# Kernel tuning notes

Hardware: AMD Instinct MI355X
Metric: run time of the kernel (lower is better)

Reference implementation:

```python
import jax, jax.numpy as jnp
import numpy as np

COMMITMENT_COST = 0.25
NUM_CODES = 1024   # module's embedding_dim arg (K)
CODE_DIM = 512     # module's num_embeddings arg (D)


def setup_inputs() -> dict:
    key = jax.random.key(0)
    k1, k2 = jax.random.split(key)
    latents = jax.random.normal(k1, (64, 512, 512), dtype=jnp.float32)
    # torch init: uniform_(-1/K, 1/K)
    codebook = jax.random.uniform(
        k2, (NUM_CODES, CODE_DIM), dtype=jnp.float32,
        minval=-1.0 / NUM_CODES, maxval=1.0 / NUM_CODES)
    return {"continous_latents": latents, "codebook": codebook}


def reference(continous_latents, codebook):
    latents_shape = continous_latents.shape
    flat = continous_latents.reshape(-1, codebook.shape[1])        # [N, D]
    # squared Euclidean distances (argmin-equivalent to torch.cdist)
    d2 = (jnp.sum(flat * flat, axis=1, keepdims=True)
          - 2.0 * flat @ codebook.T
          + jnp.sum(codebook * codebook, axis=1))                  # [N, K]
    enc_idx = jnp.argmin(d2, axis=1)                               # [N]
    quantized = codebook[enc_idx].reshape(latents_shape)           # gather == one-hot matmul
    commitment_loss = jnp.mean(
        (jax.lax.stop_gradient(quantized) - continous_latents) ** 2)
    embedding_loss = jnp.mean(
        (quantized - jax.lax.stop_gradient(continous_latents)) ** 2)
    vq_loss = embedding_loss + COMMITMENT_COST * commitment_loss
    # straight-through estimator
    quantized_st = continous_latents + jax.lax.stop_gradient(
        quantized - continous_latents)
    return (quantized_st, vq_loss)
```

## Files before the change

kernel.cpp:

```cpp
#include <hip/hip_runtime.h>
#include <cfloat>

#define LAT_ROWS 32768
#define DIM 512
#define KCODES 1024

constexpr int BM = 64;
constexpr int BN = 256;
constexpr int BK = 64;
constexpr int NT = 512;
constexpr int NCT = KCODES / BN;
constexpr int NDK = DIM / BK;
constexpr int TT = NCT * NDK;
constexpr int CUNITS = BN * BK / 8;

constexpr size_t WS_LSUM = 0;
constexpr size_t WS_NORM = 512;
constexpr size_t WS_CBF8 = 4608;
constexpr size_t WS_XF8  = 4608 + 524288;
constexpr size_t WS_NEEDED = WS_XF8 + (size_t)LAT_ROWS * DIM;

typedef float f32x4 __attribute__((ext_vector_type(4)));
typedef short bf16x8 __attribute__((ext_vector_type(8)));
typedef unsigned short u16;
typedef u16 u16x8 __attribute__((ext_vector_type(8)));

__device__ __forceinline__ u16 f2bf(float f) {
  unsigned u = __float_as_uint(f);
  u += 0x7FFF + ((u >> 16) & 1);
  return (u16)(u >> 16);
}

__device__ __forceinline__ int2 pk8_fp8(const float4 a, const float4 c) {
  int lo = __builtin_amdgcn_cvt_pk_fp8_f32(a.x, a.y, 0, false);
  lo = __builtin_amdgcn_cvt_pk_fp8_f32(a.z, a.w, lo, true);
  int hi = __builtin_amdgcn_cvt_pk_fp8_f32(c.x, c.y, 0, false);
  hi = __builtin_amdgcn_cvt_pk_fp8_f32(c.z, c.w, hi, true);
  int2 v; v.x = lo; v.y = hi;
  return v;
}

#define GLOAD_LDS(g, l)                                     \
  __builtin_amdgcn_global_load_lds(                         \
      (const __attribute__((address_space(1))) void*)(g),   \
      (__attribute__((address_space(3))) void*)(l), 16, 0, 0)

__global__ void __launch_bounds__(NT)
vq_prep(const float* __restrict__ X, const float* __restrict__ CB,
        long* __restrict__ Xf8, long* __restrict__ CBf8,
        float* __restrict__ norms, double* __restrict__ lsum) {
  __shared__ float sp[8];
  const int bb = blockIdx.x;
  const int tid = threadIdx.x;
  if (bb < 4096) {
    const int id = bb * NT + tid;
    const int l15 = id & 15;
    const int l4 = (id >> 4) & 3;
    const int ks = (id >> 6) & 1;
    const int nf = (id >> 7) & 1;
    const int wn = (id >> 8) & 1;
    const int dk = (id >> 9) & 7;
    const int b = id >> 12;
    const int r = b * 64 + wn * 32 + nf * 16 + l15;
    const int d0 = dk * 64 + ks * 32 + l4 * 8;
    const float* src = X + (size_t)r * DIM + d0;
    const float4 a = *(const float4*)src;
    const float4 c = *(const float4*)(src + 4);
    float s = a.x * a.x + a.y * a.y + a.z * a.z + a.w * a.w +
              c.x * c.x + c.y * c.y + c.z * c.z + c.w * c.w;
    *(int2*)(Xf8 + id) = pk8_fp8(a, c);
#pragma unroll
    for (int m = 1; m < 64; m <<= 1) s += __shfl_xor(s, m, 64);
    const int lane = tid & 63, w = tid >> 6;
    if (lane == 0) sp[w] = s;
    __syncthreads();
    if (tid == 0) {
      double t = 0.0;
      for (int i = 0; i < 8; ++i) t += (double)sp[i];
      atomicAdd(&lsum[bb & 63], t);
    }
  } else if (bb < 4224) {
    const int id = (bb - 4096) * NT + tid;
    const int ct = id >> 14;
    const int dk = (id >> 11) & 7;
    const int u = id & 2047;
    const int r = u >> 3, qp = u & 7, q = qp ^ (r & 7);
    const float* src = CB + ((size_t)ct * BN + r) * DIM + dk * BK + q * 8;
    const float4 a = *(const float4*)src;
    const float4 c = *(const float4*)(src + 4);
    *(int2*)(CBf8 + id) = pk8_fp8(a, c);
  } else {
    const int gw = (bb - 4224) * 8 + (tid >> 6);
    const int l = tid & 63;
    const float4 a = *(const float4*)&CB[(size_t)gw * DIM + l * 8];
    const float4 b = *(const float4*)&CB[(size_t)gw * DIM + l * 8 + 4];
    float s = a.x * a.x + a.y * a.y + a.z * a.z + a.w * a.w +
              b.x * b.x + b.y * b.y + b.z * b.z + b.w * b.w;
#pragma unroll
    for (int m = 1; m < 64; m <<= 1) s += __shfl_xor(s, m, 64);
    if (l == 0) norms[gw] = s;
  }
}

__global__ void __launch_bounds__(NT, 4)
vq_main9(const long* __restrict__ Xf8, const long* __restrict__ CBf8,
         const float* __restrict__ CB, const float* __restrict__ norms,
         float* __restrict__ outq, double* __restrict__ lsum) {
  __shared__ long Cs[2][CUNITS];
  __shared__ float snorm[KCODES];
  __shared__ float redm[BM][4];
  __shared__ int redi[BM][4];
  __shared__ int idxs[BM];
  __shared__ float wpart[8];

  const int tid = threadIdx.x;
  const int lane = tid & 63;
  const int l15 = lane & 15;
  const int l4 = lane >> 4;
  const int wid = tid >> 6;
  const int wm = wid & 3;
  const int wn = wid >> 2;
  const int b = blockIdx.x;
  const int row0 = b * BM;

  for (int i = tid; i < KCODES; i += NT) snorm[i] = norms[i];

  const long* xw = Xf8 + (size_t)b * 4096 + wn * 256 + lane;

  auto stage = [&](int bf, int t) {
    const int ct = t >> 3, dk = t & 7;
    const char* cp = (const char*)(CBf8 + (size_t)(ct * NDK + dk) * CUNITS);
    char* dst = (char*)&Cs[bf][0];
#pragma unroll
    for (int k = 0; k < 2; ++k) {
      const int o = (tid + k * NT) * 16;
      GLOAD_LDS(cp + o, dst + o);
    }
  };

  f32x4 acc[4][2];
  float rmin[2]; int ridx[2];
#pragma unroll
  for (int i = 0; i < 2; ++i) { rmin[i] = FLT_MAX; ridx[i] = 0; }

  stage(0, 0);
  __syncthreads();

  for (int t = 0; t < TT; ++t) {
    const int dk = t & 7;
    const int cur = t & 1;
    long bfr[2][2];
    const long* xp = xw + dk * 512;
#pragma unroll
    for (int ks = 0; ks < 2; ++ks)
#pragma unroll
      for (int nf = 0; nf < 2; ++nf)
        bfr[ks][nf] = xp[nf * 128 + ks * 64];
    if (t + 1 < TT) stage(cur ^ 1, t + 1);

    if (dk == 0) {
      const f32x4 z = {0.f, 0.f, 0.f, 0.f};
#pragma unroll
      for (int mf = 0; mf < 4; ++mf)
#pragma unroll
        for (int nf = 0; nf < 2; ++nf) acc[mf][nf] = z;
    }
#pragma unroll
    for (int ks = 0; ks < 2; ++ks) {
      long af[4];
#pragma unroll
      for (int mf = 0; mf < 4; ++mf) {
        const int r = wm * 64 + mf * 16 + l15;
        const int ph = (ks * 4 + l4) ^ (r & 7);
        af[mf] = Cs[cur][r * 8 + ph];
      }
      __builtin_amdgcn_s_setprio(1);
#pragma unroll
      for (int mf = 0; mf < 4; ++mf)
#pragma unroll
        for (int nf = 0; nf < 2; ++nf)
          acc[mf][nf] = __builtin_amdgcn_mfma_f32_16x16x32_fp8_fp8(
              af[mf], bfr[ks][nf], acc[mf][nf], 0, 0, 0);
      __builtin_amdgcn_s_setprio(0);
    }
    if (dk == NDK - 1) {
      const int ct = t >> 3;
#pragma unroll
      for (int mf = 0; mf < 4; ++mf) {
#pragma unroll
        for (int r = 0; r < 4; ++r) {
          const int code = ct * BN + wm * 64 + mf * 16 + l4 * 4 + r;
          const float cn = snorm[code];
#pragma unroll
          for (int nf = 0; nf < 2; ++nf) {
            const float s = fmaf(-2.f, acc[mf][nf][r], cn);
            if (s < rmin[nf]) { rmin[nf] = s; ridx[nf] = code; }
          }
        }
      }
    }
    __syncthreads();
  }

#pragma unroll
  for (int m = 16; m <= 32; m <<= 1) {
#pragma unroll
    for (int nf = 0; nf < 2; ++nf) {
      const float om = __shfl_xor(rmin[nf], m, 64);
      const int oi = __shfl_xor(ridx[nf], m, 64);
      if (om < rmin[nf] || (om == rmin[nf] && oi < ridx[nf])) {
        rmin[nf] = om; ridx[nf] = oi;
      }
    }
  }
  if (l4 == 0) {
#pragma unroll
    for (int nf = 0; nf < 2; ++nf) {
      const int row = wn * 32 + nf * 16 + l15;
      redm[row][wm] = rmin[nf];
      redi[row][wm] = ridx[nf];
    }
  }
  __syncthreads();

  float tot = 0.f;
  if (tid < BM) {
    float bm = redm[tid][0]; int bi = redi[tid][0];
#pragma unroll
    for (int c = 1; c < 4; ++c) {
      const float m_ = redm[tid][c]; const int i_ = redi[tid][c];
      if (m_ < bm || (m_ == bm && i_ < bi)) { bm = m_; bi = i_; }
    }
    idxs[tid] = bi;
    tot = bm;
  }
#pragma unroll
  for (int m = 1; m < 64; m <<= 1) tot += __shfl_xor(tot, m, 64);
  if (lane == 0) wpart[wid] = tot;
  __syncthreads();
  if (tid == 0) {
    double s = 0.0;
    for (int i = 0; i < 8; ++i) s += (double)wpart[i];
    atomicAdd(&lsum[blockIdx.x & 63], s);
  }

  for (int g = tid; g < BM * (DIM / 4); g += NT) {
    const int row = g >> 7;
    const int d4 = (g & 127) * 4;
    const int idx = idxs[row];
    *(float4*)&outq[(size_t)(row0 + row) * DIM + d4] =
        *(const float4*)&CB[(size_t)idx * DIM + d4];
  }
}

constexpr int FBM = 128, FBN = 256, FBK = 64, FNT = 512, FNDK = 8, FTT = 32;

__global__ void __launch_bounds__(FNT, 2)
vq_main_fb(const float* __restrict__ X, const float* __restrict__ CB,
           const float* __restrict__ norms, float* __restrict__ outq,
           double* __restrict__ lsum) {
  __shared__ u16 Xs[2][FBM * FBK];
  __shared__ u16 Cs[2][FBN * FBK];
  __shared__ float snorm[KCODES];
  __shared__ float redm[FBM][4];
  __shared__ int redi[FBM][4];
  __shared__ int idxs[FBM];
  __shared__ float wpart[8];

  const int tid = threadIdx.x;
  const int lane = tid & 63;
  const int l15 = lane & 15;
  const int l4 = lane >> 4;
  const int wid = tid >> 6;
  const int wm = wid & 3;
  const int wn = wid >> 2;
  const int row0 = blockIdx.x * FBM;

  for (int i = tid; i < KCODES; i += FNT) snorm[i] = norms[i];

  int xlds[2]; const float* xbase[2];
#pragma unroll
  for (int k = 0; k < 2; ++k) {
    const int u = tid + k * FNT;
    const int r = u >> 3, q = u & 7, ph = q ^ (r & 7);
    xlds[k] = r * FBK + ph * 8;
    xbase[k] = X + (size_t)(row0 + r) * DIM + q * 8;
  }
  int clds[4]; const float* cbase[4];
#pragma unroll
  for (int k = 0; k < 4; ++k) {
    const int u = tid + k * FNT;
    const int r = u >> 3, q = u & 7, ph = q ^ (r & 7);
    clds[k] = r * FBK + ph * 8;
    cbase[k] = CB + (size_t)r * DIM + q * 8;
  }

  f32x4 acc[4][4];
  float rmin[4]; int ridx[4];
#pragma unroll
  for (int i = 0; i < 4; ++i) { rmin[i] = FLT_MAX; ridx[i] = 0; }
  float sq = 0.f;

  float4 lx[2][2], lc[4][2];
  auto load_tile = [&](int tn) {
    const int ct = tn >> 3, dk = tn & 7;
    const int xo = dk * FBK;
    const size_t co = (size_t)ct * FBN * DIM + dk * FBK;
#pragma unroll
    for (int k = 0; k < 2; ++k) {
      lx[k][0] = *(const float4*)(xbase[k] + xo);
      lx[k][1] = *(const float4*)(xbase[k] + xo + 4);
    }
#pragma unroll
    for (int k = 0; k < 4; ++k) {
      lc[k][0] = *(const float4*)(cbase[k] + co);
      lc[k][1] = *(const float4*)(cbase[k] + co + 4);
    }
  };
  auto write_tile = [&](int bb, bool acc_sq) {
#pragma unroll
    for (int k = 0; k < 2; ++k) {
      u16x8 v;
      const float* f = (const float*)&lx[k][0];
#pragma unroll
      for (int j = 0; j < 8; ++j) {
        const float x = f[j];
        if (acc_sq) sq = fmaf(x, x, sq);
        v[j] = f2bf(x);
      }
      *(u16x8*)&Xs[bb][xlds[k]] = v;
    }
#pragma unroll
    for (int k = 0; k < 4; ++k) {
      u16x8 v;
      const float* f = (const float*)&lc[k][0];
#pragma unroll
      for (int j = 0; j < 8; ++j) v[j] = f2bf(f[j]);
      *(u16x8*)&Cs[bb][clds[k]] = v;
    }
  };

  load_tile(0);
  write_tile(0, true);
  __syncthreads();

  int cur = 0;
  for (int t = 0; t < FTT; ++t) {
    const int dk = t & 7;
    const bool pre = (t + 1 < FTT);
    if (pre) load_tile(t + 1);
    if (dk == 0) {
      const f32x4 z = {0.f, 0.f, 0.f, 0.f};
#pragma unroll
      for (int mf = 0; mf < 4; ++mf)
#pragma unroll
        for (int nf = 0; nf < 4; ++nf) acc[mf][nf] = z;
    }
    const u16* xb = Xs[cur];
    const u16* cb = Cs[cur];
#pragma unroll
    for (int ks = 0; ks < 2; ++ks) {
      bf16x8 af[4], bfr[4];
#pragma unroll
      for (int mf = 0; mf < 4; ++mf) {
        const int r = wm * 64 + mf * 16 + l15;
        const int ph = (ks * 4 + l4) ^ (r & 7);
        af[mf] = *(const bf16x8*)&cb[r * FBK + ph * 8];
      }
#pragma unroll
      for (int nf = 0; nf < 4; ++nf) {
        const int r = wn * 64 + nf * 16 + l15;
        const int ph = (ks * 4 + l4) ^ (r & 7);
        bfr[nf] = *(const bf16x8*)&xb[r * FBK + ph * 8];
      }
#pragma unroll
      for (int mf = 0; mf < 4; ++mf)
#pragma unroll
        for (int nf = 0; nf < 4; ++nf)
          acc[mf][nf] = __builtin_amdgcn_mfma_f32_16x16x32_bf16(
              af[mf], bfr[nf], acc[mf][nf], 0, 0, 0);
    }
    if (dk == FNDK - 1) {
      const int ct = t >> 3;
#pragma unroll
      for (int mf = 0; mf < 4; ++mf) {
#pragma unroll
        for (int r = 0; r < 4; ++r) {
          const int code = ct * FBN + wm * 64 + mf * 16 + l4 * 4 + r;
          const float cn = snorm[code];
#pragma unroll
          for (int nf = 0; nf < 4; ++nf) {
            const float s = fmaf(-2.f, acc[mf][nf][r], cn);
            if (s < rmin[nf]) { rmin[nf] = s; ridx[nf] = code; }
          }
        }
      }
    }
    if (pre) write_tile(cur ^ 1, (t + 1) < FNDK);
    __syncthreads();
    cur ^= 1;
  }

#pragma unroll
  for (int m = 16; m <= 32; m <<= 1) {
#pragma unroll
    for (int nf = 0; nf < 4; ++nf) {
      const float om = __shfl_xor(rmin[nf], m, 64);
      const int oi = __shfl_xor(ridx[nf], m, 64);
      if (om < rmin[nf] || (om == rmin[nf] && oi < ridx[nf])) {
        rmin[nf] = om; ridx[nf] = oi;
      }
    }
  }
  if (l4 == 0) {
#pragma unroll
    for (int nf = 0; nf < 4; ++nf) {
      const int row = wn * 64 + nf * 16 + l15;
      redm[row][wm] = rmin[nf];
      redi[row][wm] = ridx[nf];
    }
  }
  __syncthreads();

  float tot = sq;
  if (tid < FBM) {
    float bm = redm[tid][0]; int bi = redi[tid][0];
#pragma unroll
    for (int c = 1; c < 4; ++c) {
      const float m_ = redm[tid][c]; const int i_ = redi[tid][c];
      if (m_ < bm || (m_ == bm && i_ < bi)) { bm = m_; bi = i_; }
    }
    idxs[tid] = bi;
    tot += bm;
  }
#pragma unroll
  for (int m = 1; m < 64; m <<= 1) tot += __shfl_xor(tot, m, 64);
  if (lane == 0) wpart[wid] = tot;
  __syncthreads();
  if (tid == 0) {
    double s = 0.0;
    for (int i = 0; i < 8; ++i) s += (double)wpart[i];
    atomicAdd(&lsum[blockIdx.x & 63], s);
  }

  for (int g = tid; g < FBM * (DIM / 4); g += FNT) {
    const int row = g >> 7;
    const int d4 = (g & 127) * 4;
    const int idx = idxs[row];
    *(float4*)&outq[(size_t)(row0 + row) * DIM + d4] =
        *(const float4*)&CB[(size_t)idx * DIM + d4];
  }
}

__global__ void vq_norms_kernel(const float* __restrict__ cb,
                                float* __restrict__ norms) {
  const int gw = (int)((blockIdx.x * blockDim.x + threadIdx.x) >> 6);
  const int l = threadIdx.x & 63;
  const float4 a = *(const float4*)&cb[(size_t)gw * DIM + l * 8];
  const float4 b = *(const float4*)&cb[(size_t)gw * DIM + l * 8 + 4];
  float s = a.x * a.x + a.y * a.y + a.z * a.z + a.w * a.w +
            b.x * b.x + b.y * b.y + b.z * b.z + b.w * b.w;
#pragma unroll
  for (int m = 1; m < 64; m <<= 1) s += __shfl_xor(s, m, 64);
  if (l == 0) norms[gw] = s;
}

__global__ void vq_finalize_kernel(const double* __restrict__ lsum,
                                   float* __restrict__ out) {
  double t = 0.0;
  for (int i = 0; i < 64; ++i) t += lsum[i];
  out[0] = (float)(1.25 * t / (double)((size_t)LAT_ROWS * DIM));
}

extern "C" void kernel_launch(void* const* d_in, const int* in_sizes, int n_in,
                              void* d_out, int out_size, void* d_ws, size_t ws_size,
                              hipStream_t stream) {
  const float* X = (const float*)d_in[0];
  const float* CB = (const float*)d_in[1];
  float* out = (float*)d_out;
  double* lsum = (double*)((char*)d_ws + WS_LSUM);
  float* norms = (float*)((char*)d_ws + WS_NORM);

  hipMemsetAsync(d_ws, 0, 512, stream);
  if (ws_size >= WS_NEEDED) {
    long* CBf8 = (long*)((char*)d_ws + WS_CBF8);
    long* Xf8 = (long*)((char*)d_ws + WS_XF8);
    vq_prep<<<4352, NT, 0, stream>>>(X, CB, Xf8, CBf8, norms, lsum);
    vq_main9<<<LAT_ROWS / BM, NT, 0, stream>>>(Xf8, CBf8, CB, norms, out, lsum);
  } else {
    vq_norms_kernel<<<KCODES / 4, 256, 0, stream>>>(CB, norms);
    vq_main_fb<<<LAT_ROWS / FBM, FNT, 0, stream>>>(X, CB, norms, out, lsum);
  }
  vq_finalize_kernel<<<1, 1, 0, stream>>>(lsum, out + (size_t)LAT_ROWS * DIM);
}
```

Baseline: 69.01 us.

## Double K-step per barrier in main loop and coalesce fp8 prep via LDS

The main kernel now stages two 64-wide K slices of the fp8 codebook per pipeline phase, which halves the number of barriers and stage calls while doubling LDS usage for the codebook buffer. The LDS swizzle changes from an XOR on the row to a rotation keyed on the lane's row index, and the codebook prep writes its layout to match. The latent prep kernel now has each block convert a whole 64-row tile with coalesced reads, permutes it through padded shared memory, and writes the fragment layout out contiguously, which cuts the block count from 4096 to 512. The larger LDS footprint could reduce occupancy.

```diff
diff --git a/kernel.cpp b/kernel.cpp
--- a/kernel.cpp
+++ b/kernel.cpp
@@ -11,7 +11,7 @@
 constexpr int NT = 512;
 constexpr int NCT = KCODES / BN;
 constexpr int NDK = DIM / BK;
-constexpr int TT = NCT * NDK;
+constexpr int NPH = 16;
 constexpr int CUNITS = BN * BK / 8;
 
 constexpr size_t WS_LSUM = 0;
@@ -49,26 +49,35 @@
 vq_prep(const float* __restrict__ X, const float* __restrict__ CB,
         long* __restrict__ Xf8, long* __restrict__ CBf8,
         float* __restrict__ norms, double* __restrict__ lsum) {
-  __shared__ float sp[8];
   const int bb = blockIdx.x;
   const int tid = threadIdx.x;
-  if (bb < 4096) {
-    const int id = bb * NT + tid;
-    const int l15 = id & 15;
-    const int l4 = (id >> 4) & 3;
-    const int ks = (id >> 6) & 1;
-    const int nf = (id >> 7) & 1;
-    const int wn = (id >> 8) & 1;
-    const int dk = (id >> 9) & 7;
-    const int b = id >> 12;
-    const int r = b * 64 + wn * 32 + nf * 16 + l15;
-    const int d0 = dk * 64 + ks * 32 + l4 * 8;
-    const float* src = X + (size_t)r * DIM + d0;
-    const float4 a = *(const float4*)src;
-    const float4 c = *(const float4*)(src + 4);
-    float s = a.x * a.x + a.y * a.y + a.z * a.z + a.w * a.w +
-              c.x * c.x + c.y * c.y + c.z * c.z + c.w * c.w;
-    *(int2*)(Xf8 + id) = pk8_fp8(a, c);
+  if (bb < 512) {
+    __shared__ long xl[4096 + 256];
+    __shared__ float sp[8];
+    float s = 0.f;
+#pragma unroll
+    for (int c = 0; c < 8; ++c) {
+      const int j = c * NT + tid;
+      const int r = j >> 6;
+      const int d0 = (j & 63) * 8;
+      const float* src = X + ((size_t)bb * BM + r) * DIM + d0;
+      const float4 a = *(const float4*)src;
+      const float4 cc = *(const float4*)(src + 4);
+      s += a.x * a.x + a.y * a.y + a.z * a.z + a.w * a.w +
+           cc.x * cc.x + cc.y * cc.y + cc.z * cc.z + cc.w * cc.w;
+      const int dk = d0 >> 6, ks = (d0 >> 5) & 1, l4 = (d0 >> 3) & 3;
+      const int wn = (r >> 5) & 1, nf = (r >> 4) & 1, l15 = r & 15;
+      const int unit = dk * 512 + wn * 256 + nf * 128 + ks * 64 + l4 * 16 + l15;
+      const int2 v = pk8_fp8(a, cc);
+      *(int2*)&xl[unit + (unit >> 4)] = v;
+    }
+    __syncthreads();
+    long* dst = Xf8 + (size_t)bb * 4096;
+#pragma unroll
+    for (int k = 0; k < 8; ++k) {
+      const int u = k * NT + tid;
+      dst[u] = xl[u + (u >> 4)];
+    }
 #pragma unroll
     for (int m = 1; m < 64; m <<= 1) s += __shfl_xor(s, m, 64);
     const int lane = tid & 63, w = tid >> 6;
@@ -79,18 +88,19 @@
       for (int i = 0; i < 8; ++i) t += (double)sp[i];
       atomicAdd(&lsum[bb & 63], t);
     }
-  } else if (bb < 4224) {
-    const int id = (bb - 4096) * NT + tid;
+  } else if (bb < 640) {
+    const int id = (bb - 512) * NT + tid;
     const int ct = id >> 14;
     const int dk = (id >> 11) & 7;
     const int u = id & 2047;
-    const int r = u >> 3, qp = u & 7, q = qp ^ (r & 7);
+    const int r = u >> 3, qp = u & 7;
+    const int q = (qp + 8 - ((r >> 1) & 7)) & 7;
     const float* src = CB + ((size_t)ct * BN + r) * DIM + dk * BK + q * 8;
     const float4 a = *(const float4*)src;
     const float4 c = *(const float4*)(src + 4);
     *(int2*)(CBf8 + id) = pk8_fp8(a, c);
   } else {
-    const int gw = (bb - 4224) * 8 + (tid >> 6);
+    const int gw = (bb - 640) * 8 + (tid >> 6);
     const int l = tid & 63;
     const float4 a = *(const float4*)&CB[(size_t)gw * DIM + l * 8];
     const float4 b = *(const float4*)&CB[(size_t)gw * DIM + l * 8 + 4];
@@ -103,10 +113,10 @@
 }
 
 __global__ void __launch_bounds__(NT, 4)
-vq_main9(const long* __restrict__ Xf8, const long* __restrict__ CBf8,
-         const float* __restrict__ CB, const float* __restrict__ norms,
-         float* __restrict__ outq, double* __restrict__ lsum) {
-  __shared__ long Cs[2][CUNITS];
+vq_main10(const long* __restrict__ Xf8, const long* __restrict__ CBf8,
+          const float* __restrict__ CB, const float* __restrict__ norms,
+          float* __restrict__ outq, double* __restrict__ lsum) {
+  __shared__ long Cs[2][2 * CUNITS];
   __shared__ float snorm[KCODES];
   __shared__ float redm[BM][4];
   __shared__ int redi[BM][4];
@@ -127,12 +137,12 @@
 
   const long* xw = Xf8 + (size_t)b * 4096 + wn * 256 + lane;
 
-  auto stage = [&](int bf, int t) {
-    const int ct = t >> 3, dk = t & 7;
-    const char* cp = (const char*)(CBf8 + (size_t)(ct * NDK + dk) * CUNITS);
+  auto stage = [&](int bf, int tt) {
+    const int ct = tt >> 2, pr = tt & 3;
+    const char* cp = (const char*)(CBf8 + (size_t)(ct * NDK + pr * 2) * CUNITS);
     char* dst = (char*)&Cs[bf][0];
 #pragma unroll
-    for (int k = 0; k < 2; ++k) {
+    for (int k = 0; k < 4; ++k) {
       const int o = (tid + k * NT) * 16;
       GLOAD_LDS(cp + o, dst + o);
     }
@@ -146,19 +156,22 @@
   stage(0, 0);
   __syncthreads();
 
-  for (int t = 0; t < TT; ++t) {
-    const int dk = t & 7;
-    const int cur = t & 1;
-    long bfr[2][2];
-    const long* xp = xw + dk * 512;
-#pragma unroll
-    for (int ks = 0; ks < 2; ++ks)
-#pragma unroll
-      for (int nf = 0; nf < 2; ++nf)
-        bfr[ks][nf] = xp[nf * 128 + ks * 64];
-    if (t + 1 < TT) stage(cur ^ 1, t + 1);
-
-    if (dk == 0) {
+  for (int tt = 0; tt < NPH; ++tt) {
+    const int pr = tt & 3;
+    const int cur = tt & 1;
+    long bfr[2][2][2];
+#pragma unroll
+    for (int dkp = 0; dkp < 2; ++dkp) {
+      const long* xp = xw + (pr * 2 + dkp) * 512;
+#pragma unroll
+      for (int ks = 0; ks < 2; ++ks)
+#pragma unroll
+        for (int nf = 0; nf < 2; ++nf)
+          bfr[dkp][ks][nf] = xp[nf * 128 + ks * 64];
+    }
+    if (tt + 1 < NPH) stage(cur ^ 1, tt + 1);
+
+    if (pr == 0) {
       const f32x4 z = {0.f, 0.f, 0.f, 0.f};
 #pragma unroll
       for (int mf = 0; mf < 4; ++mf)
@@ -166,25 +179,28 @@
         for (int nf = 0; nf < 2; ++nf) acc[mf][nf] = z;
     }
 #pragma unroll
-    for (int ks = 0; ks < 2; ++ks) {
-      long af[4];
-#pragma unroll
-      for (int mf = 0; mf < 4; ++mf) {
-        const int r = wm * 64 + mf * 16 + l15;
-        const int ph = (ks * 4 + l4) ^ (r & 7);
-        af[mf] = Cs[cur][r * 8 + ph];
-      }
-      __builtin_amdgcn_s_setprio(1);
-#pragma unroll
-      for (int mf = 0; mf < 4; ++mf)
-#pragma unroll
-        for (int nf = 0; nf < 2; ++nf)
-          acc[mf][nf] = __builtin_amdgcn_mfma_f32_16x16x32_fp8_fp8(
-              af[mf], bfr[ks][nf], acc[mf][nf], 0, 0, 0);
-      __builtin_amdgcn_s_setprio(0);
-    }
-    if (dk == NDK - 1) {
-      const int ct = t >> 3;
+    for (int dkp = 0; dkp < 2; ++dkp) {
+#pragma unroll
+      for (int ks = 0; ks < 2; ++ks) {
+        long af[4];
+#pragma unroll
+        for (int mf = 0; mf < 4; ++mf) {
+          const int r = wm * 64 + mf * 16 + l15;
+          const int ph = ((ks * 4 + l4) + (l15 >> 1)) & 7;
+          af[mf] = Cs[cur][dkp * CUNITS + r * 8 + ph];
+        }
+        __builtin_amdgcn_s_setprio(1);
+#pragma unroll
+        for (int mf = 0; mf < 4; ++mf)
+#pragma unroll
+          for (int nf = 0; nf < 2; ++nf)
+            acc[mf][nf] = __builtin_amdgcn_mfma_f32_16x16x32_fp8_fp8(
+                af[mf], bfr[dkp][ks][nf], acc[mf][nf], 0, 0, 0);
+        __builtin_amdgcn_s_setprio(0);
+      }
+    }
+    if (pr == 3) {
+      const int ct = tt >> 2;
 #pragma unroll
       for (int mf = 0; mf < 4; ++mf) {
 #pragma unroll
@@ -485,8 +501,8 @@
   if (ws_size >= WS_NEEDED) {
     long* CBf8 = (long*)((char*)d_ws + WS_CBF8);
     long* Xf8 = (long*)((char*)d_ws + WS_XF8);
-    vq_prep<<<4352, NT, 0, stream>>>(X, CB, Xf8, CBf8, norms, lsum);
-    vq_main9<<<LAT_ROWS / BM, NT, 0, stream>>>(Xf8, CBf8, CB, norms, out, lsum);
+    vq_prep<<<768, NT, 0, stream>>>(X, CB, Xf8, CBf8, norms, lsum);
+    vq_main10<<<LAT_ROWS / BM, NT, 0, stream>>>(Xf8, CBf8, CB, norms, out, lsum);
   } else {
     vq_norms_kernel<<<KCODES / 4, 256, 0, stream>>>(CB, norms);
     vq_main_fb<<<LAT_ROWS / FBM, FNT, 0, stream>>>(X, CB, norms, out, lsum);
```

After: 65.15 us. 5.6% less time.

## Fuse latent FP8 conversion into main kernel, stream codebook from global

Applied to the files above, without the earlier changes.

Drops the separate pass that converted all latents to FP8 in workspace. The main kernel now reads its 64-row fp32 tile of X directly, converts it to FP8 in a swizzled LDS layout, and accumulates the latent squared norm on the fly. Codebook fragments, pre-packed in MFMA register order, are loaded straight from global memory (L2-resident) instead of double-buffered through LDS, which removes the per-step barriers. This saves the 64 MB intermediate write and read, at the cost of exposing global-load latency inside the MFMA loop.

```diff
diff --git a/kernel.cpp b/kernel.cpp
--- a/kernel.cpp
+++ b/kernel.cpp
@@ -7,18 +7,14 @@
 
 constexpr int BM = 64;
 constexpr int BN = 256;
-constexpr int BK = 64;
 constexpr int NT = 512;
-constexpr int NCT = KCODES / BN;
-constexpr int NDK = DIM / BK;
-constexpr int TT = NCT * NDK;
-constexpr int CUNITS = BN * BK / 8;
+constexpr int NCT = 4;
+constexpr int NDK = 8;
 
 constexpr size_t WS_LSUM = 0;
 constexpr size_t WS_NORM = 512;
 constexpr size_t WS_CBF8 = 4608;
-constexpr size_t WS_XF8  = 4608 + 524288;
-constexpr size_t WS_NEEDED = WS_XF8 + (size_t)LAT_ROWS * DIM;
+constexpr size_t WS_NEEDED = WS_CBF8 + 65536 * 8;
 
 typedef float f32x4 __attribute__((ext_vector_type(4)));
 typedef short bf16x8 __attribute__((ext_vector_type(8)));
@@ -31,66 +27,39 @@
   return (u16)(u >> 16);
 }
 
-__device__ __forceinline__ int2 pk8_fp8(const float4 a, const float4 c) {
+__device__ __forceinline__ long pk8_fp8l(const float4 a, const float4 c) {
   int lo = __builtin_amdgcn_cvt_pk_fp8_f32(a.x, a.y, 0, false);
   lo = __builtin_amdgcn_cvt_pk_fp8_f32(a.z, a.w, lo, true);
   int hi = __builtin_amdgcn_cvt_pk_fp8_f32(c.x, c.y, 0, false);
   hi = __builtin_amdgcn_cvt_pk_fp8_f32(c.z, c.w, hi, true);
-  int2 v; v.x = lo; v.y = hi;
-  return v;
-}
-
-#define GLOAD_LDS(g, l)                                     \
-  __builtin_amdgcn_global_load_lds(                         \
-      (const __attribute__((address_space(1))) void*)(g),   \
-      (__attribute__((address_space(3))) void*)(l), 16, 0, 0)
+  return ((long)(unsigned)hi << 32) | (unsigned)lo;
+}
+
+__device__ __forceinline__ int xswz(int u) {
+  const int add = ((u >> 2) & 12) + ((u >> 5) & 2) + ((u >> 9) & 1);
+  return (u & ~15) | ((u + add) & 15);
+}
 
 __global__ void __launch_bounds__(NT)
-vq_prep(const float* __restrict__ X, const float* __restrict__ CB,
-        long* __restrict__ Xf8, long* __restrict__ CBf8,
-        float* __restrict__ norms, double* __restrict__ lsum) {
-  __shared__ float sp[8];
+vq_prep11(const float* __restrict__ CB, long* __restrict__ CBf8,
+          float* __restrict__ norms) {
   const int bb = blockIdx.x;
   const int tid = threadIdx.x;
-  if (bb < 4096) {
+  if (bb < 128) {
     const int id = bb * NT + tid;
-    const int l15 = id & 15;
-    const int l4 = (id >> 4) & 3;
-    const int ks = (id >> 6) & 1;
-    const int nf = (id >> 7) & 1;
-    const int wn = (id >> 8) & 1;
-    const int dk = (id >> 9) & 7;
-    const int b = id >> 12;
-    const int r = b * 64 + wn * 32 + nf * 16 + l15;
-    const int d0 = dk * 64 + ks * 32 + l4 * 8;
-    const float* src = X + (size_t)r * DIM + d0;
+    const int t = id >> 11;
+    const int r = id & 2047;
+    const int wm = r >> 9, mf = (r >> 7) & 3, ks = (r >> 6) & 1,
+              l4 = (r >> 4) & 3, l15 = id & 15;
+    const int ct = t >> 3, dk = t & 7;
+    const int code = ct * BN + wm * 64 + mf * 16 + l15;
+    const int d0 = dk * 64 + (ks * 4 + l4) * 8;
+    const float* src = CB + (size_t)code * DIM + d0;
     const float4 a = *(const float4*)src;
     const float4 c = *(const float4*)(src + 4);
-    float s = a.x * a.x + a.y * a.y + a.z * a.z + a.w * a.w +
-              c.x * c.x + c.y * c.y + c.z * c.z + c.w * c.w;
-    *(int2*)(Xf8 + id) = pk8_fp8(a, c);
-#pragma unroll
-    for (int m = 1; m < 64; m <<= 1) s += __shfl_xor(s, m, 64);
-    const int lane = tid & 63, w = tid >> 6;
-    if (lane == 0) sp[w] = s;
-    __syncthreads();
-    if (tid == 0) {
-      double t = 0.0;
-      for (int i = 0; i < 8; ++i) t += (double)sp[i];
-      atomicAdd(&lsum[bb & 63], t);
-    }
-  } else if (bb < 4224) {
-    const int id = (bb - 4096) * NT + tid;
-    const int ct = id >> 14;
-    const int dk = (id >> 11) & 7;
-    const int u = id & 2047;
-    const int r = u >> 3, qp = u & 7, q = qp ^ (r & 7);
-    const float* src = CB + ((size_t)ct * BN + r) * DIM + dk * BK + q * 8;
-    const float4 a = *(const float4*)src;
-    const float4 c = *(const float4*)(src + 4);
-    *(int2*)(CBf8 + id) = pk8_fp8(a, c);
+    CBf8[id] = pk8_fp8l(a, c);
   } else {
-    const int gw = (bb - 4224) * 8 + (tid >> 6);
+    const int gw = (bb - 128) * 8 + (tid >> 6);
     const int l = tid & 63;
     const float4 a = *(const float4*)&CB[(size_t)gw * DIM + l * 8];
     const float4 b = *(const float4*)&CB[(size_t)gw * DIM + l * 8 + 4];
@@ -103,10 +72,10 @@
 }
 
 __global__ void __launch_bounds__(NT, 4)
-vq_main9(const long* __restrict__ Xf8, const long* __restrict__ CBf8,
-         const float* __restrict__ CB, const float* __restrict__ norms,
-         float* __restrict__ outq, double* __restrict__ lsum) {
-  __shared__ long Cs[2][CUNITS];
+vq_main11(const float* __restrict__ X, const long* __restrict__ CBf8,
+          const float* __restrict__ CB, const float* __restrict__ norms,
+          float* __restrict__ outq, double* __restrict__ lsum) {
+  __shared__ long Xs[4096];
   __shared__ float snorm[KCODES];
   __shared__ float redm[BM][4];
   __shared__ int redi[BM][4];
@@ -125,40 +94,29 @@
 
   for (int i = tid; i < KCODES; i += NT) snorm[i] = norms[i];
 
-  const long* xw = Xf8 + (size_t)b * 4096 + wn * 256 + lane;
-
-  auto stage = [&](int bf, int t) {
-    const int ct = t >> 3, dk = t & 7;
-    const char* cp = (const char*)(CBf8 + (size_t)(ct * NDK + dk) * CUNITS);
-    char* dst = (char*)&Cs[bf][0];
-#pragma unroll
-    for (int k = 0; k < 2; ++k) {
-      const int o = (tid + k * NT) * 16;
-      GLOAD_LDS(cp + o, dst + o);
-    }
-  };
+  float sq = 0.f;
+#pragma unroll
+  for (int c = 0; c < 8; ++c) {
+    const int rl = c * 8 + wid;
+    const float* src = X + (size_t)(row0 + rl) * DIM + lane * 8;
+    const float4 a = *(const float4*)src;
+    const float4 d = *(const float4*)(src + 4);
+    sq += a.x * a.x + a.y * a.y + a.z * a.z + a.w * a.w +
+          d.x * d.x + d.y * d.y + d.z * d.z + d.w * d.w;
+    const int q = lane;
+    const int u = (q >> 3) * 512 + (rl >> 5) * 256 + ((rl >> 4) & 1) * 128 +
+                  ((q >> 2) & 1) * 64 + (q & 3) * 16 + (rl & 15);
+    Xs[xswz(u)] = pk8_fp8l(a, d);
+  }
+  __syncthreads();
 
   f32x4 acc[4][2];
   float rmin[2]; int ridx[2];
 #pragma unroll
   for (int i = 0; i < 2; ++i) { rmin[i] = FLT_MAX; ridx[i] = 0; }
 
-  stage(0, 0);
-  __syncthreads();
-
-  for (int t = 0; t < TT; ++t) {
-    const int dk = t & 7;
-    const int cur = t & 1;
-    long bfr[2][2];
-    const long* xp = xw + dk * 512;
-#pragma unroll
-    for (int ks = 0; ks < 2; ++ks)
-#pragma unroll
-      for (int nf = 0; nf < 2; ++nf)
-        bfr[ks][nf] = xp[nf * 128 + ks * 64];
-    if (t + 1 < TT) stage(cur ^ 1, t + 1);
-
-    if (dk == 0) {
+  for (int ct = 0; ct < NCT; ++ct) {
+    {
       const f32x4 z = {0.f, 0.f, 0.f, 0.f};
 #pragma unroll
       for (int mf = 0; mf < 4; ++mf)
@@ -166,40 +124,46 @@
         for (int nf = 0; nf < 2; ++nf) acc[mf][nf] = z;
     }
 #pragma unroll
-    for (int ks = 0; ks < 2; ++ks) {
-      long af[4];
-#pragma unroll
-      for (int mf = 0; mf < 4; ++mf) {
-        const int r = wm * 64 + mf * 16 + l15;
-        const int ph = (ks * 4 + l4) ^ (r & 7);
-        af[mf] = Cs[cur][r * 8 + ph];
-      }
+    for (int dk = 0; dk < NDK; ++dk) {
+      const long* cbt = CBf8 + ((ct * 8 + dk) * 2048 + wm * 512) + lane;
+      long af[2][4];
+#pragma unroll
+      for (int ks = 0; ks < 2; ++ks)
+#pragma unroll
+        for (int mf = 0; mf < 4; ++mf)
+          af[ks][mf] = cbt[mf * 128 + ks * 64];
+      long bfr[2][2];
+#pragma unroll
+      for (int ks = 0; ks < 2; ++ks)
+#pragma unroll
+        for (int nf = 0; nf < 2; ++nf) {
+          const int u = dk * 512 + wn * 256 + nf * 128 + ks * 64 + l4 * 16 + l15;
+          bfr[ks][nf] = Xs[xswz(u)];
+        }
       __builtin_amdgcn_s_setprio(1);
 #pragma unroll
-      for (int mf = 0; mf < 4; ++mf)
-#pragma unroll
-        for (int nf = 0; nf < 2; ++nf)
-          acc[mf][nf] = __builtin_amdgcn_mfma_f32_16x16x32_fp8_fp8(
-              af[mf], bfr[ks][nf], acc[mf][nf], 0, 0, 0);
+      for (int ks = 0; ks < 2; ++ks)
+#pragma unroll
+        for (int mf = 0; mf < 4; ++mf)
+#pragma unroll
+          for (int nf = 0; nf < 2; ++nf)
+            acc[mf][nf] = __builtin_amdgcn_mfma_f32_16x16x32_fp8_fp8(
+                af[ks][mf], bfr[ks][nf], acc[mf][nf], 0, 0, 0);
       __builtin_amdgcn_s_setprio(0);
     }
-    if (dk == NDK - 1) {
-      const int ct = t >> 3;
-#pragma unroll
-      for (int mf = 0; mf < 4; ++mf) {
-#pragma unroll
-        for (int r = 0; r < 4; ++r) {
-          const int code = ct * BN + wm * 64 + mf * 16 + l4 * 4 + r;
-          const float cn = snorm[code];
-#pragma unroll
-          for (int nf = 0; nf < 2; ++nf) {
-            const float s = fmaf(-2.f, acc[mf][nf][r], cn);
-            if (s < rmin[nf]) { rmin[nf] = s; ridx[nf] = code; }
-          }
+#pragma unroll
+    for (int mf = 0; mf < 4; ++mf) {
+#pragma unroll
+      for (int r = 0; r < 4; ++r) {
+        const int code = ct * BN + wm * 64 + mf * 16 + l4 * 4 + r;
+        const float cn = snorm[code];
+#pragma unroll
+        for (int nf = 0; nf < 2; ++nf) {
+          const float s = fmaf(-2.f, acc[mf][nf][r], cn);
+          if (s < rmin[nf]) { rmin[nf] = s; ridx[nf] = code; }
         }
       }
     }
-    __syncthreads();
   }
 
 #pragma unroll
@@ -223,7 +187,7 @@
   }
   __syncthreads();
 
-  float tot = 0.f;
+  float tot = sq;
   if (tid < BM) {
     float bm = redm[tid][0]; int bi = redi[tid][0];
 #pragma unroll
@@ -232,7 +196,7 @@
       if (m_ < bm || (m_ == bm && i_ < bi)) { bm = m_; bi = i_; }
     }
     idxs[tid] = bi;
-    tot = bm;
+    tot += bm;
   }
 #pragma unroll
   for (int m = 1; m < 64; m <<= 1) tot += __shfl_xor(tot, m, 64);
@@ -241,7 +205,7 @@
   if (tid == 0) {
     double s = 0.0;
     for (int i = 0; i < 8; ++i) s += (double)wpart[i];
-    atomicAdd(&lsum[blockIdx.x & 63], s);
+    atomicAdd(&lsum[b & 63], s);
   }
 
   for (int g = tid; g < BM * (DIM / 4); g += NT) {
@@ -484,9 +448,8 @@
   hipMemsetAsync(d_ws, 0, 512, stream);
   if (ws_size >= WS_NEEDED) {
     long* CBf8 = (long*)((char*)d_ws + WS_CBF8);
-    long* Xf8 = (long*)((char*)d_ws + WS_XF8);
-    vq_prep<<<4352, NT, 0, stream>>>(X, CB, Xf8, CBf8, norms, lsum);
-    vq_main9<<<LAT_ROWS / BM, NT, 0, stream>>>(Xf8, CBf8, CB, norms, out, lsum);
+    vq_prep11<<<256, NT, 0, stream>>>(CB, CBf8, norms);
+    vq_main11<<<LAT_ROWS / BM, NT, 0, stream>>>(X, CBf8, CB, norms, out, lsum);
   } else {
     vq_norms_kernel<<<KCODES / 4, 256, 0, stream>>>(CB, norms);
     vq_main_fb<<<LAT_ROWS / FBM, FNT, 0, stream>>>(X, CB, norms, out, lsum);
```

Measured after the change: 83.98 us. +21.7%, slower.
